# Kernel optimization log

Hardware: AMD Instinct MI355X
Metric: run time of the kernel (lower is better)

Reference implementation:

```python
import jax, jax.numpy as jnp
import numpy as np

B, IN, H = 8192, 512, 512


def _binarize(w):
    # sign() forward with straight-through gradient (ebnn Binarize)
    return w + jax.lax.stop_gradient(jnp.sign(w) - w)


def setup_inputs() -> dict:
    key = jax.random.key(0)
    ks = jax.random.split(key, 7)
    stdv = 1.0 / np.sqrt(H)
    return {
        "x": jax.random.normal(ks[0], (B, IN), jnp.float32),
        "hx": jax.random.normal(ks[1], (B, H), jnp.float32),
        "cx": jax.random.normal(ks[2], (B, H), jnp.float32),
        "W_ih": jax.random.uniform(ks[3], (4 * H, IN), jnp.float32, -stdv, stdv),
        "W_hh": jax.random.uniform(ks[4], (4 * H, H), jnp.float32, -stdv, stdv),
        "bias_ih": jax.random.uniform(ks[5], (4 * H,), jnp.float32, -stdv, stdv),
        "bias_hh": jax.random.uniform(ks[6], (4 * H,), jnp.float32, -stdv, stdv),
    }


def reference(x, hx, cx, W_ih, W_hh, bias_ih, bias_hh):
    # gates: [B, 4H] = x @ sign(W_ih)^T + b_ih + hx @ sign(W_hh)^T + b_hh
    gates = (jnp.einsum("bi,gi->bg", x, _binarize(W_ih)) + bias_ih
             + jnp.einsum("bh,gh->bg", hx, _binarize(W_hh)) + bias_hh)
    ingate, forgetgate, cellgate, outgate = jnp.split(gates, 4, axis=1)
    cy = jax.nn.sigmoid(forgetgate) * cx + jax.nn.sigmoid(ingate) * jnp.tanh(cellgate)
    hy = jax.nn.sigmoid(outgate) * jnp.tanh(cy)
    return (hy, cy)
```

## Files before the change

kernel.cpp:

```cpp
#include <hip/hip_runtime.h>
#include <hip/hip_bf16.h>
#include <stdint.h>


typedef __attribute__((ext_vector_type(4))) int int4x;
typedef __attribute__((ext_vector_type(4))) float float4x;

#define B_DIM 8192
#define H_DIM 512

__device__ __forceinline__ float bf2f(uint16_t u) {
  return __uint_as_float(((uint32_t)u) << 16);
}
__device__ __forceinline__ uint16_t f2bf(float f) {
  uint32_t u = __float_as_uint(f);
  return (uint16_t)((u + 0x7FFFu + ((u >> 16) & 1u)) >> 16);
}
__device__ __forceinline__ float sigm(float x) { return 1.0f / (1.0f + __expf(-x)); }
__device__ __forceinline__ float tanh_f(float x) { return 2.0f / (1.0f + __expf(-2.0f * x)) - 1.0f; }

__device__ __forceinline__ int detect_f32(const void* x) {
  const int l = threadIdx.x & 63;
  uint32_t wrd = ((const uint32_t*)x)[l];
  uint32_t e0 = (wrd >> 7) & 0xFFu, e1 = (wrd >> 23) & 0xFFu;
  return __ballot(e0 > 0x85u || e1 > 0x85u) != 0ull;
}

__device__ __forceinline__ void quant4(const float* v, uint32_t* hi4, uint32_t* lo4) {
  uint32_t h = 0, lo = 0;
#pragma unroll
  for (int j = 0; j < 4; ++j) {
    float c = fminf(fmaxf(v[j], -8.0f), 8.0f);
    int xf = __float2int_rn(c * 4096.0f);
    xf = xf > 32639 ? 32639 : xf;
    xf = xf < -32768 ? -32768 : xf;
    const int lb = (xf << 24) >> 24;
    const int hb = (xf - lb) >> 8;
    lo |= ((uint32_t)lb & 0xFFu) << (8 * j);
    h |= ((uint32_t)hb & 0xFFu) << (8 * j);
  }
  *hi4 = h;
  *lo4 = lo;
}

__global__ __launch_bounds__(256) void prep_kernel(
    const void* __restrict__ x, const void* __restrict__ hx,
    const void* __restrict__ w_ih, const void* __restrict__ w_hh,
    int8_t* __restrict__ Xhi, int8_t* __restrict__ Xlo, int8_t* __restrict__ Bp) {
  __shared__ alignas(16) char lsc[33280];
  const int isF32 = detect_f32(x);
  const int t = threadIdx.x;
  const int w = t >> 6, l = t & 63;
  const int isX = blockIdx.x < 512;
  const int grp = isX ? blockIdx.x : (blockIdx.x - 512);

#pragma unroll
  for (int rr = 0; rr < 4; ++rr) {
    const int r = w * 4 + rr;
    long rowbase;
    if (isX) rowbase = (long)(grp * 16 + r) * 512;
    else     rowbase = (long)((grp & 3) * 512 + (grp >> 2) * 16 + r) * 512;
#pragma unroll
    for (int src = 0; src < 2; ++src) {
      const void* sp_ = isX ? (src ? hx : x) : (src ? w_hh : w_ih);
#pragma unroll
      for (int q = 0; q < 2; ++q) {
        const int k = src * 512 + q * 256 + l * 4;
        float v[4];
        if (isF32) {
          float4x f = *(const float4x*)((const float*)sp_ + rowbase + q * 256 + l * 4);
          v[0] = f[0]; v[1] = f[1]; v[2] = f[2]; v[3] = f[3];
        } else {
          const uint16_t* s = (const uint16_t*)sp_ + rowbase + q * 256 + l * 4;
#pragma unroll
          for (int j = 0; j < 4; ++j) v[j] = bf2f(s[j]);
        }
        if (isX) {
          uint32_t h4, lo4;
          quant4(v, &h4, &lo4);
          *(uint32_t*)(lsc + r * 1040 + k) = h4;
          *(uint32_t*)(lsc + 16640 + r * 1040 + k) = lo4;
        } else {
          uint32_t s4 = 0;
#pragma unroll
          for (int j = 0; j < 4; ++j) {
            const int sv = v[j] > 0.f ? 1 : (v[j] < 0.f ? -1 : 0);
            s4 |= ((uint32_t)sv & 0xFFu) << (8 * j);
          }
          *(uint32_t*)(lsc + r * 1040 + k) = s4;
        }
      }
    }
  }
  __syncthreads();
  const int kt = t >> 4, quad = (t >> 2) & 3, rb = (t & 3) * 4;
  const int loff = kt * 64 + quad * 16;
  if (isX) {
    int4x h[4], lo[4];
#pragma unroll
    for (int i = 0; i < 4; ++i) {
      h[i] = *(const int4x*)(lsc + (rb + i) * 1040 + loff);
      lo[i] = *(const int4x*)(lsc + 16640 + (rb + i) * 1040 + loff);
    }
    int4x* dh = (int4x*)(Xhi + (long)grp * 16384 + t * 64);
    int4x* dl = (int4x*)(Xlo + (long)grp * 16384 + t * 64);
#pragma unroll
    for (int i = 0; i < 4; ++i) { dh[i] = h[i]; dl[i] = lo[i]; }
  } else {
    int4x s[4];
#pragma unroll
    for (int i = 0; i < 4; ++i)
      s[i] = *(const int4x*)(lsc + (rb + i) * 1040 + loff);
    int4x* db = (int4x*)(Bp + (long)grp * 16384 + t * 64);
#pragma unroll
    for (int i = 0; i < 4; ++i) db[i] = s[i];
  }
}

__global__ __launch_bounds__(512, 2) void blstm_gemm_kernel(
    const int8_t* __restrict__ Xhi, const int8_t* __restrict__ Xlo,
    const int8_t* __restrict__ Bp, const void* __restrict__ b_ih,
    const void* __restrict__ b_hh, const void* __restrict__ cx,
    const void* __restrict__ xdet, void* __restrict__ out) {
  __shared__ alignas(16) char lds[65536];
  const int tid = threadIdx.x;
  const int l = tid & 63, w = tid >> 6;
  const int lrow = l & 15, lq = l >> 4;
  const int wy = w >> 1, wx = w & 1;
  const int isF32 = detect_f32(xdet);
  const int bid = blockIdx.x;
  const int rt = (bid & 7) * 4 + (bid >> 7);
  const int bx = (bid >> 3) & 15;

  const int8_t* aph[4];
  const int8_t* apl[4];
#pragma unroll
  for (int mt = 0; mt < 4; ++mt) {
    const long off = ((long)(rt * 16 + wy * 4 + mt) << 14) + l * 16;
    aph[mt] = Xhi + off;
    apl[mt] = Xlo + off;
  }
  const int8_t* bsrc = Bp + ((long)(bx * 8) << 14) + tid * 16;

  int4x acch[4][4], accl[4][4];
#pragma unroll
  for (int mt = 0; mt < 4; ++mt)
#pragma unroll
    for (int g = 0; g < 4; ++g) {
      acch[mt][g] = (int4x){0, 0, 0, 0};
      accl[mt][g] = (int4x){0, 0, 0, 0};
    }

  int4x ah[2][4], al[2][4];
#pragma unroll
  for (int mt = 0; mt < 4; ++mt) {
    ah[0][mt] = *(const int4x*)aph[mt]; aph[mt] += 1024;
    al[0][mt] = *(const int4x*)apl[mt]; apl[mt] += 1024;
  }
#pragma unroll
  for (int g = 0; g < 8; ++g)
    *(int4x*)(lds + g * 8192 + tid * 16) = *(const int4x*)(bsrc + g * 16384);
  asm volatile("s_waitcnt lgkmcnt(0)\n\ts_barrier" ::: "memory");

#pragma unroll
  for (int ks = 0; ks < 16; ++ks) {
    const int cur = ks & 1, nxt = cur ^ 1;
    if (ks == 8) {
      asm volatile("s_waitcnt lgkmcnt(0)\n\ts_barrier" ::: "memory");
#pragma unroll
      for (int g = 0; g < 8; ++g)
        *(int4x*)(lds + g * 8192 + tid * 16) = *(const int4x*)(bsrc + g * 16384 + 8192);
      asm volatile("s_waitcnt lgkmcnt(0)\n\ts_barrier" ::: "memory");
    }
    if (ks < 15) {
#pragma unroll
      for (int mt = 0; mt < 4; ++mt) {
        ah[nxt][mt] = *(const int4x*)aph[mt]; aph[mt] += 1024;
        al[nxt][mt] = *(const int4x*)apl[mt]; apl[mt] += 1024;
      }
    }
    int4x b[4];
#pragma unroll
    for (int g = 0; g < 4; ++g)
      b[g] = *(const int4x*)(lds + (wx * 4 + g) * 8192 + (ks & 7) * 1024 + l * 16);
    __builtin_amdgcn_s_setprio(1);
#pragma unroll
    for (int mt = 0; mt < 4; ++mt)
#pragma unroll
      for (int g = 0; g < 4; ++g) {
        acch[mt][g] = __builtin_amdgcn_mfma_i32_16x16x64_i8(ah[cur][mt], b[g], acch[mt][g], 0, 0, 0);
        accl[mt][g] = __builtin_amdgcn_mfma_i32_16x16x64_i8(al[cur][mt], b[g], accl[mt][g], 0, 0, 0);
      }
    __builtin_amdgcn_s_setprio(0);
  }

  const long CYo = (long)B_DIM * H_DIM;
  const int c = bx * 32 + wx * 16 + lrow;
  float biasv[4];
#pragma unroll
  for (int g = 0; g < 4; ++g) {
    if (isF32)
      biasv[g] = ((const float*)b_ih)[g * 512 + c] + ((const float*)b_hh)[g * 512 + c];
    else
      biasv[g] = bf2f(((const uint16_t*)b_ih)[g * 512 + c]) + bf2f(((const uint16_t*)b_hh)[g * 512 + c]);
  }
  float* outF = (float*)out;
  uint16_t* outB = (uint16_t*)out;
#pragma unroll
  for (int mt = 0; mt < 4; ++mt) {
#pragma unroll
    for (int r = 0; r < 4; ++r) {
      const int row = rt * 256 + wy * 64 + mt * 16 + lq * 4 + r;
      const long cidx = (long)row * H_DIM + c;
      float vg[4];
#pragma unroll
      for (int g = 0; g < 4; ++g)
        vg[g] = fmaf((float)acch[mt][g][r], 0.0625f,
                     fmaf((float)accl[mt][g][r], 2.44140625e-4f, biasv[g]));
      const float cxv = isF32 ? ((const float*)cx)[cidx] : bf2f(((const uint16_t*)cx)[cidx]);
      const float ig = sigm(vg[0]), fg = sigm(vg[1]), og = sigm(vg[3]);
      const float cg = tanh_f(vg[2]);
      const float cy = fg * cxv + ig * cg;
      const float hy = og * tanh_f(cy);
      if (isF32) {
        outF[cidx] = hy;
        outF[CYo + cidx] = cy;
      } else {
        outB[cidx] = f2bf(hy);
        outB[CYo + cidx] = f2bf(cy);
      }
    }
  }
}

extern "C" void kernel_launch(void* const* d_in, const int* in_sizes, int n_in,
                              void* d_out, int out_size, void* d_ws, size_t ws_size,
                              hipStream_t stream) {
  const void* x = d_in[0];
  const void* hx = d_in[1];
  const void* cx = d_in[2];
  const void* W_ih = d_in[3];
  const void* W_hh = d_in[4];
  const void* b_ih = d_in[5];
  const void* b_hh = d_in[6];
  char* ws = (char*)d_ws;
  int8_t* Xhi = (int8_t*)ws;
  int8_t* Xlo = (int8_t*)(ws + 8388608);
  int8_t* Bp = (int8_t*)(ws + 16777216);

  prep_kernel<<<640, 256, 0, stream>>>(x, hx, W_ih, W_hh, Xhi, Xlo, Bp);
  blstm_gemm_kernel<<<512, 512, 0, stream>>>(Xhi, Xlo, Bp, b_ih, b_hh, cx, x, d_out);
}
```

Before: 172.7 us.

## Stage A and B tiles through LDS with triple-buffered async global_load_lds

The GEMM kernel now uses 256-thread blocks with 128-row tiles over a 1024-block grid. Both the hi/lo activation tiles and the binarized weight tiles are staged into LDS with direct global-to-LDS loads, using a three-stage ring buffer that prefetches two K-steps ahead. Previously A was loaded straight into registers and B was reloaded into LDS in two halves behind barriers. This is meant to overlap memory latency with MFMA work, at the cost of a barrier every K-step, more LDS per block and smaller tiles that reload B more often.

```diff
diff --git a/kernel.cpp b/kernel.cpp
--- a/kernel.cpp
+++ b/kernel.cpp
@@ -41,6 +41,12 @@
   }
   *hi4 = h;
   *lo4 = lo;
+}
+
+__device__ __forceinline__ void gload16(const void* g, void* l) {
+  __builtin_amdgcn_global_load_lds(
+      (const __attribute__((address_space(1))) unsigned int*)g,
+      (__attribute__((address_space(3))) unsigned int*)l, 16, 0, 0);
 }
 
 __global__ __launch_bounds__(256) void prep_kernel(
@@ -117,30 +123,38 @@
   }
 }
 
-__global__ __launch_bounds__(512, 2) void blstm_gemm_kernel(
+__global__ __launch_bounds__(256, 2) void blstm_gemm_kernel(
     const int8_t* __restrict__ Xhi, const int8_t* __restrict__ Xlo,
     const int8_t* __restrict__ Bp, const void* __restrict__ b_ih,
     const void* __restrict__ b_hh, const void* __restrict__ cx,
     const void* __restrict__ xdet, void* __restrict__ out) {
-  __shared__ alignas(16) char lds[65536];
+  __shared__ alignas(16) char lds[73728];
   const int tid = threadIdx.x;
   const int l = tid & 63, w = tid >> 6;
   const int lrow = l & 15, lq = l >> 4;
   const int wy = w >> 1, wx = w & 1;
   const int isF32 = detect_f32(xdet);
   const int bid = blockIdx.x;
-  const int rt = (bid & 7) * 4 + (bid >> 7);
-  const int bx = (bid >> 3) & 15;
-
-  const int8_t* aph[4];
-  const int8_t* apl[4];
-#pragma unroll
-  for (int mt = 0; mt < 4; ++mt) {
-    const long off = ((long)(rt * 16 + wy * 4 + mt) << 14) + l * 16;
-    aph[mt] = Xhi + off;
-    apl[mt] = Xlo + off;
-  }
-  const int8_t* bsrc = Bp + ((long)(bx * 8) << 14) + tid * 16;
+  const int idx = bid >> 3;
+  const int by = (bid & 7) * 8 + (idx >> 4);
+  const int bx = idx & 15;
+
+  const int8_t* csrc[6];
+  int cdst[6];
+#pragma unroll
+  for (int i = 0; i < 6; ++i) {
+    const int c = w * 6 + i;
+    if (c < 8) {
+      csrc[i] = Xhi + (((long)(by * 8 + c)) << 14) + l * 16;
+      cdst[i] = c * 1024;
+    } else if (c < 16) {
+      csrc[i] = Xlo + (((long)(by * 8 + (c - 8))) << 14) + l * 16;
+      cdst[i] = 8192 + (c - 8) * 1024;
+    } else {
+      csrc[i] = Bp + (((long)(bx * 8 + (c - 16))) << 14) + l * 16;
+      cdst[i] = 16384 + (c - 16) * 1024;
+    }
+  }
 
   int4x acch[4][4], accl[4][4];
 #pragma unroll
@@ -151,47 +165,43 @@
       accl[mt][g] = (int4x){0, 0, 0, 0};
     }
 
-  int4x ah[2][4], al[2][4];
-#pragma unroll
-  for (int mt = 0; mt < 4; ++mt) {
-    ah[0][mt] = *(const int4x*)aph[mt]; aph[mt] += 1024;
-    al[0][mt] = *(const int4x*)apl[mt]; apl[mt] += 1024;
-  }
-#pragma unroll
-  for (int g = 0; g < 8; ++g)
-    *(int4x*)(lds + g * 8192 + tid * 16) = *(const int4x*)(bsrc + g * 16384);
-  asm volatile("s_waitcnt lgkmcnt(0)\n\ts_barrier" ::: "memory");
+#pragma unroll
+  for (int i = 0; i < 6; ++i) gload16(csrc[i], lds + cdst[i]);
+#pragma unroll
+  for (int i = 0; i < 6; ++i) gload16(csrc[i] + 1024, lds + 24576 + cdst[i]);
+  asm volatile("s_waitcnt vmcnt(6)\n\ts_barrier" ::: "memory");
 
 #pragma unroll
   for (int ks = 0; ks < 16; ++ks) {
-    const int cur = ks & 1, nxt = cur ^ 1;
-    if (ks == 8) {
-      asm volatile("s_waitcnt lgkmcnt(0)\n\ts_barrier" ::: "memory");
-#pragma unroll
-      for (int g = 0; g < 8; ++g)
-        *(int4x*)(lds + g * 8192 + tid * 16) = *(const int4x*)(bsrc + g * 16384 + 8192);
-      asm volatile("s_waitcnt lgkmcnt(0)\n\ts_barrier" ::: "memory");
-    }
-    if (ks < 15) {
-#pragma unroll
-      for (int mt = 0; mt < 4; ++mt) {
-        ah[nxt][mt] = *(const int4x*)aph[mt]; aph[mt] += 1024;
-        al[nxt][mt] = *(const int4x*)apl[mt]; apl[mt] += 1024;
-      }
-    }
-    int4x b[4];
+    const int cb = (ks % 3) * 24576;
+    if (ks < 14) {
+      const int nb = ((ks + 2) % 3) * 24576;
+#pragma unroll
+      for (int i = 0; i < 6; ++i)
+        gload16(csrc[i] + (long)(ks + 2) * 1024, lds + nb + cdst[i]);
+    }
+    int4x ah[4], al[4], b[4];
+#pragma unroll
+    for (int mt = 0; mt < 4; ++mt) {
+      ah[mt] = *(const int4x*)(lds + cb + (wy * 4 + mt) * 1024 + l * 16);
+      al[mt] = *(const int4x*)(lds + cb + 8192 + (wy * 4 + mt) * 1024 + l * 16);
+    }
 #pragma unroll
     for (int g = 0; g < 4; ++g)
-      b[g] = *(const int4x*)(lds + (wx * 4 + g) * 8192 + (ks & 7) * 1024 + l * 16);
+      b[g] = *(const int4x*)(lds + cb + 16384 + (wx * 4 + g) * 1024 + l * 16);
     __builtin_amdgcn_s_setprio(1);
 #pragma unroll
     for (int mt = 0; mt < 4; ++mt)
 #pragma unroll
       for (int g = 0; g < 4; ++g) {
-        acch[mt][g] = __builtin_amdgcn_mfma_i32_16x16x64_i8(ah[cur][mt], b[g], acch[mt][g], 0, 0, 0);
-        accl[mt][g] = __builtin_amdgcn_mfma_i32_16x16x64_i8(al[cur][mt], b[g], accl[mt][g], 0, 0, 0);
+        acch[mt][g] = __builtin_amdgcn_mfma_i32_16x16x64_i8(ah[mt], b[g], acch[mt][g], 0, 0, 0);
+        accl[mt][g] = __builtin_amdgcn_mfma_i32_16x16x64_i8(al[mt], b[g], accl[mt][g], 0, 0, 0);
       }
     __builtin_amdgcn_s_setprio(0);
+    if (ks < 14)
+      asm volatile("s_waitcnt vmcnt(6)\n\ts_waitcnt lgkmcnt(0)\n\ts_barrier" ::: "memory");
+    else if (ks == 14)
+      asm volatile("s_waitcnt vmcnt(0)\n\ts_waitcnt lgkmcnt(0)\n\ts_barrier" ::: "memory");
   }
 
   const long CYo = (long)B_DIM * H_DIM;
@@ -210,7 +220,7 @@
   for (int mt = 0; mt < 4; ++mt) {
 #pragma unroll
     for (int r = 0; r < 4; ++r) {
-      const int row = rt * 256 + wy * 64 + mt * 16 + lq * 4 + r;
+      const int row = by * 128 + wy * 64 + mt * 16 + lq * 4 + r;
       const long cidx = (long)row * H_DIM + c;
       float vg[4];
 #pragma unroll
@@ -249,5 +259,5 @@
   int8_t* Bp = (int8_t*)(ws + 16777216);
 
   prep_kernel<<<640, 256, 0, stream>>>(x, hx, W_ih, W_hh, Xhi, Xlo, Bp);
-  blstm_gemm_kernel<<<512, 512, 0, stream>>>(Xhi, Xlo, Bp, b_ih, b_hh, cx, x, d_out);
-}
+  blstm_gemm_kernel<<<1024, 256, 0, stream>>>(Xhi, Xlo, Bp, b_ih, b_hh, cx, x, d_out);
+}
```

Result: faster. 151.9 us (-12.0%).
